# Performance work log

Measured on AMD Instinct MI355X. Metric: run time of the kernel, lower is better.

## Reference

```python
import jax, jax.numpy as jnp
import numpy as np

IN_F, OUT_F, NB = 4096, 4096, 8
BS = IN_F // NB  # 512


def setup_inputs() -> dict:
    key = jax.random.key(0)
    k1, k2, k3, k4 = jax.random.split(key, 4)
    weight = jax.random.normal(k1, (OUT_F, IN_F), dtype=jnp.float32) * 0.02
    bias = jax.random.normal(k2, (OUT_F,), dtype=jnp.float32) * 0.02
    x = jax.random.normal(k3, (4, 2048, IN_F), dtype=jnp.float32)
    R_blocks = jax.random.normal(k4, (NB, BS, BS), dtype=jnp.float32) * 0.1
    return {"weight": weight, "bias": bias, "x": x, "R_blocks": R_blocks, "layer_idx": 0}


def cayley_transform(A):
    # A: [nb, bs, bs]; Q = (I - A_skew) @ inv(I + A_skew + 1e-6 I)
    bs = A.shape[-1]
    I = jnp.eye(bs, dtype=A.dtype)
    A_skew = 0.5 * (A - jnp.swapaxes(A, -2, -1))
    return jnp.matmul(I - A_skew, jnp.linalg.inv(I + A_skew + 1e-6 * I))


def reference(weight, bias, x, R_blocks, layer_idx):
    R_ortho = cayley_transform(R_blocks)  # [nb, bs, bs]
    # weight @ block_diag(R) == per-block contraction on the in_features axis
    w = weight.reshape(OUT_F, NB, BS)
    tw = jnp.einsum('onb,nbc->onc', w, R_ortho).reshape(OUT_F, IN_F)
    # F.linear: x @ tw.T + bias
    out = jnp.einsum('bsi,oi->bso', x, tw) + bias
    return out
```

## Files before the change

kernel.cpp:

```cpp
#include <hip/hip_runtime.h>
#include <hip/hip_bf16.h>


typedef unsigned short u16;
typedef __attribute__((ext_vector_type(8))) __bf16 bf16x8;
typedef __attribute__((ext_vector_type(4))) float f32x4;
typedef __attribute__((ext_vector_type(8))) unsigned short u16x8;
typedef __attribute__((ext_vector_type(4))) unsigned short u16x4;

#define C0   1.000001f
#define C1Q  2.000001f
#define AS1 __attribute__((address_space(1)))
#define AS3 __attribute__((address_space(3)))

__device__ __forceinline__ u16 f2bf(float x) {
  union { float f; unsigned u; } v; v.f = x;
  return (u16)((v.u + 0x7fffu + ((v.u >> 16) & 1u)) >> 16);
}
__device__ __forceinline__ float bf2f(u16 h) {
  union { float f; unsigned u; } v; v.u = ((unsigned)h) << 16; return v.f;
}

__device__ __forceinline__ void get_coefs(float t, float* C) {
  float lam = powf(t, 0.25f);
  float a = 2.0f / (C0 * C0 + lam);
  float e = (lam - C0 * C0) / (lam + C0 * C0);
  float sq = e * e, c1 = 2.0f / (2.0f - sq);
  C[0] = a; C[1] = 2.0f * c1; C[2] = -c1 * a;
  C[3] = 2.0f * c1 * a; C[4] = -c1 * a * a;
  e = sq / (2.0f - sq); sq = e * e;
  float c2 = 2.0f / (2.0f - sq);
  C[5] = 2.0f * c2; C[6] = -c2;
  e = sq / (2.0f - sq); sq = e * e;
  float c3 = 2.0f / (2.0f - sq);
  C[7] = 2.0f * c3; C[8] = -c3;
}

__global__ __launch_bounds__(256) void k_build_M(const float* __restrict__ R,
                                                 u16* __restrict__ Mh,
                                                 u16* __restrict__ Ml) {
  __shared__ float t1[32][33];
  const int n = blockIdx.z;
  const int tr = blockIdx.y * 32, tc = blockIdx.x * 32;
  const int ly = threadIdx.x >> 5, lx = threadIdx.x & 31;
  const float* Rb = R + (size_t)n * 262144;
  float a[4];
#pragma unroll
  for (int i = 0; i < 4; ++i) {
    a[i] = Rb[(size_t)(tr + ly + i * 8) * 512 + tc + lx];
    t1[ly + i * 8][lx] = Rb[(size_t)(tc + ly + i * 8) * 512 + tr + lx];
  }
  __syncthreads();
#pragma unroll
  for (int i = 0; i < 4; ++i) {
    const int r = tr + ly + i * 8, c = tc + lx;
    float m = 0.5f * (a[i] - t1[lx][ly + i * 8]) + (r == c ? C0 : 0.0f);
    u16 h = f2bf(m);
    const size_t idx = (size_t)n * 262144 + (size_t)r * 512 + c;
    Mh[idx] = h;
    Ml[idx] = f2bf(m - bf2f(h));
  }
}

__global__ __launch_bounds__(256) void k_init(const u16* __restrict__ Mh,
                                              const u16* __restrict__ Ml,
                                              const u16* __restrict__ G,
                                              const u16* __restrict__ G2,
                                              const u16* __restrict__ H,
                                              const float* __restrict__ part,
                                              float* __restrict__ coef,
                                              u16* __restrict__ X1,
                                              u16* __restrict__ T2) {
  __shared__ float sp[64];
  __shared__ float sc[13];
  const int n = blockIdx.x >> 7;
  if (threadIdx.x < 64) sp[threadIdx.x] = part[n * 64 + threadIdx.x];
  __syncthreads();
  if (threadIdx.x == 0) {
    float s = 0.f;
    for (int i = 0; i < 64; ++i) s += sp[i];
    float C[9];
    get_coefs(s, C);
#pragma unroll
    for (int k = 0; k < 9; ++k) sc[k] = C[k];
    sc[9]  = 2.0f * C0 * C[3];
    sc[10] = -C[3];
    sc[11] = 2.0f * C0 * C[4];
    sc[12] = -C[4];
    coef[n] = C[0];
    coef[8 + n]  = C[1]; coef[16 + n] = C[2];
    coef[24 + n] = C[3]; coef[32 + n] = C[4];
    coef[40 + n] = C[5]; coef[48 + n] = C[6];
    coef[56 + n] = C[7]; coef[64 + n] = C[8];
  }
  __syncthreads();
  const size_t base = ((size_t)blockIdx.x * 256 + threadIdx.x) * 8;
  const int r  = (int)((base >> 9) & 511);
  const int c0 = (int)(base & 511);
  u16x8 mh = *reinterpret_cast<const u16x8*>(Mh + base);
  u16x8 ml = *reinterpret_cast<const u16x8*>(Ml + base);
  u16x8 g  = *reinterpret_cast<const u16x8*>(G  + base);
  u16x8 g2 = *reinterpret_cast<const u16x8*>(G2 + base);
  u16x8 hh = *reinterpret_cast<const u16x8*>(H  + base);
  u16x8 x1, t2;
#pragma unroll
  for (int e = 0; e < 8; ++e) {
    float m = bf2f(mh[e]) + bf2f(ml[e]);
    float gv = bf2f(g[e]);
    x1[e] = f2bf((r == c0 + e ? sc[9] : 0.0f) + sc[10] * m + sc[11] * gv +
                 sc[12] * bf2f(hh[e]));
    t2[e] = f2bf(sc[3] * gv + sc[4] * bf2f(g2[e]));
  }
  *reinterpret_cast<u16x8*>(X1 + base) = x1;
  *reinterpret_cast<u16x8*>(T2 + base) = t2;
}

#define BMM_FRAGS(rs)                                                          \
  bf16x8 a[2], b[2], al2[2], bl2[2];                                           \
  _Pragma("unroll")                                                            \
  for (int i = 0; i < 2; ++i) {                                                \
    const int fr = wr * 32 + i * 16 + c15;                                     \
    const int ia = (rs) * 2048 + fr * 32 + ((lk ^ (fr & 3)) * 8);              \
    a[i] = *reinterpret_cast<const bf16x8*>(&sA[ia]);                          \
    if constexpr (PROD3) al2[i] = *reinterpret_cast<const bf16x8*>(&sAl[ia]);  \
  }                                                                            \
  _Pragma("unroll")                                                            \
  for (int j = 0; j < 2; ++j) {                                                \
    const int fc = wc * 32 + j * 16 + c15;                                     \
    const int ib = (rs) * 2048 + fc * 32 + ((lk ^ (fc & 3)) * 8);              \
    b[j] = *reinterpret_cast<const bf16x8*>(&sB[ib]);                          \
    if constexpr (PROD3) bl2[j] = *reinterpret_cast<const bf16x8*>(&sBl[ib]);  \
  }                                                                            \
  _Pragma("unroll")                                                            \
  for (int i = 0; i < 2; ++i)                                                  \
    _Pragma("unroll")                                                          \
    for (int j = 0; j < 2; ++j) {                                              \
      acc[i][j] = __builtin_amdgcn_mfma_f32_16x16x32_bf16(a[i], b[j], acc[i][j], 0, 0, 0); \
      if constexpr (PROD3) {                                                   \
        acc[i][j] = __builtin_amdgcn_mfma_f32_16x16x32_bf16(a[i],   bl2[j], acc[i][j], 0, 0, 0); \
        acc[i][j] = __builtin_amdgcn_mfma_f32_16x16x32_bf16(al2[i], b[j],   acc[i][j], 0, 0, 0); \
      }                                                                        \
    }

#define BMM_WAIT(SEL)                                                          \
  if ((SEL) == 0) {                                                            \
    if constexpr (PROD3) asm volatile("s_waitcnt vmcnt(12)" ::: "memory");     \
    else                 asm volatile("s_waitcnt vmcnt(6)" ::: "memory");      \
  } else if ((SEL) == 1) {                                                     \
    if constexpr (PROD3) asm volatile("s_waitcnt vmcnt(8)" ::: "memory");      \
    else                 asm volatile("s_waitcnt vmcnt(4)" ::: "memory");      \
  } else if ((SEL) == 2) {                                                     \
    if constexpr (PROD3) asm volatile("s_waitcnt vmcnt(4)" ::: "memory");      \
    else                 asm volatile("s_waitcnt vmcnt(2)" ::: "memory");      \
  } else {                                                                     \
    asm volatile("s_waitcnt vmcnt(0)" ::: "memory");                           \
  }

template <int PROD3, int DMODE, int OMODE, int DUAL, int FROB, int VOUT = 0>
__global__ __launch_bounds__(256)
void k_bmm(const u16* __restrict__ Ah, const u16* __restrict__ Al,
           const u16* __restrict__ Bh, const u16* __restrict__ Bl,
           const u16* __restrict__ Dh, const u16* __restrict__ Dl,
           u16* __restrict__ Cnh, u16* __restrict__ Cnl,
           u16* __restrict__ Cth, u16* __restrict__ Ctl,
           float cd, float cs,
           const float* __restrict__ cdp, const float* __restrict__ csp,
           const float* __restrict__ cvsrc, u16* __restrict__ cvdst, int zmm,
           const u16* __restrict__ A2, const u16* __restrict__ B2,
           const u16* __restrict__ D2, u16* __restrict__ C2,
           float* __restrict__ part) {
  __shared__ __align__(16) u16 sA[5 * 2048], sB[5 * 2048];
  __shared__ __align__(16) u16 sAl[PROD3 ? 5 * 2048 : 8];
  __shared__ __align__(16) u16 sBl[PROD3 ? 5 * 2048 : 8];
  __shared__ float fred[FROB ? 4 : 1];

  if ((int)blockIdx.z >= zmm) {
    const int zi = ((int)blockIdx.z - zmm) * 64 + blockIdx.y * 8 + blockIdx.x;
    const int chunk = zi >> 7;
    const int base = (zi & 127) * 256 + (int)threadIdx.x;
    const float* src = cvsrc + (size_t)chunk * 4194304;
    u16* dst = cvdst + (size_t)chunk * 4194304;
#pragma unroll
    for (int e = 0; e < 16; ++e) {
      const size_t g = (size_t)(base + e * 32768) * 8;
      float4 f0 = *reinterpret_cast<const float4*>(src + g);
      float4 f1 = *reinterpret_cast<const float4*>(src + g + 4);
      u16x8 w;
      w[0] = f2bf(f0.x); w[1] = f2bf(f0.y); w[2] = f2bf(f0.z); w[3] = f2bf(f0.w);
      w[4] = f2bf(f1.x); w[5] = f2bf(f1.y); w[6] = f2bf(f1.z); w[7] = f2bf(f1.w);
      *reinterpret_cast<u16x8*>(dst + g) = w;
    }
    return;
  }

  const int zq = DUAL ? ((blockIdx.z >> 3) & 1) : 0;
  const u16* Ah_ = (DUAL && zq) ? A2 : Ah;
  const u16* Bh_ = (DUAL && zq) ? B2 : Bh;
  const u16* Dh_ = (DUAL && zq) ? D2 : Dh;
  u16* Cnh_ = (DUAL && zq) ? C2 : Cnh;
  const size_t zb = (size_t)(blockIdx.z & 7) * 262144;
  const int tid = threadIdx.x, lane = tid & 63, wave = tid >> 6;
  const int m0 = blockIdx.y * 64, n0 = blockIdx.x * 64;
  const int wr = wave >> 1, wc = wave & 1;
  const int c15 = lane & 15, lk = lane >> 4;
  const int srow = tid >> 2;
  const int sg = (tid & 3) ^ (srow & 3);
  f32x4 acc[2][2] = {};
  const u16* pa = Ah_ + zb + (size_t)(m0 + srow) * 512 + sg * 8;
  const u16* pb = Bh_ + zb + (size_t)(n0 + srow) * 512 + sg * 8;
  const u16* pal = PROD3 ? Al + zb + (size_t)(m0 + srow) * 512 + sg * 8 : pa;
  const u16* pbl = PROD3 ? Bl + zb + (size_t)(n0 + srow) * 512 + sg * 8 : pb;

  int jn = 0, js = 0;
  auto STG = [&]() {
    if (jn < 16) {
      const int off = jn << 5;
      __builtin_amdgcn_global_load_lds((const AS1 void*)(pa + off),
                                       (AS3 void*)(sA + js * 2048 + tid * 8), 16, 0, 0);
      __builtin_amdgcn_global_load_lds((const AS1 void*)(pb + off),
                                       (AS3 void*)(sB + js * 2048 + tid * 8), 16, 0, 0);
      if constexpr (PROD3) {
        __builtin_amdgcn_global_load_lds((const AS1 void*)(pal + off),
                                         (AS3 void*)(sAl + js * 2048 + tid * 8), 16, 0, 0);
        __builtin_amdgcn_global_load_lds((const AS1 void*)(pbl + off),
                                         (AS3 void*)(sBl + js * 2048 + tid * 8), 16, 0, 0);
      }
    }
    ++jn; js = (js == 4) ? 0 : js + 1;
  };

  STG(); STG(); STG();
  int rs = 0;
  for (int t = 0; t < 13; ++t) {
    STG();
    BMM_WAIT(0)
    __builtin_amdgcn_s_barrier();
    BMM_FRAGS(rs)
    rs = (rs == 4) ? 0 : rs + 1;
  }
  STG();
  BMM_WAIT(1)
  __builtin_amdgcn_s_barrier();
  { BMM_FRAGS(rs) }
  rs = (rs == 4) ? 0 : rs + 1;
  STG();
  BMM_WAIT(2)
  __builtin_amdgcn_s_barrier();
  { BMM_FRAGS(rs) }
  rs = (rs == 4) ? 0 : rs + 1;
  STG();
  BMM_WAIT(3)
  __builtin_amdgcn_s_barrier();
  { BMM_FRAGS(rs) }

  const float cdL = cdp ? cdp[blockIdx.z & 7] : cd;
  const float csL = csp ? csp[blockIdx.z & 7] : cs;
  float fs = 0.f;
#pragma unroll
  for (int i = 0; i < 2; ++i)
#pragma unroll
    for (int j = 0; j < 2; ++j) {
      const int rowb = m0 + wr * 32 + i * 16 + lk * 4;
      const int col  = n0 + wc * 32 + j * 16 + c15;
      u16 hv[4], lv[4];
#pragma unroll
      for (int r = 0; r < 4; ++r) {
        float val = csL * acc[i][j][r];
        float dv = 0.f;
        if constexpr (DMODE >= 1) {
          dv = bf2f(Dh_[zb + (size_t)(rowb + r) * 512 + col]);
          if constexpr (DMODE == 2) dv += bf2f(Dl[zb + (size_t)(rowb + r) * 512 + col]);
        }
        float nval, tval;
        if constexpr (VOUT) { tval = val; nval = cdL * dv - val; }
        else { nval = tval = val + cdL * dv; }
        u16 nh = f2bf(nval);
        if constexpr (OMODE & 1) Cnh_[zb + (size_t)(rowb + r) * 512 + col] = nh;
        if constexpr (FROB) { float v = bf2f(nh); fs += v * v; }
        if constexpr (OMODE & 2)
          Cnl[zb + (size_t)(rowb + r) * 512 + col] = f2bf(nval - bf2f(nh));
        if constexpr (OMODE & 12) {
          u16 th = f2bf(tval);
          hv[r] = th;
          if constexpr (OMODE & 8) lv[r] = f2bf(tval - bf2f(th));
        }
      }
      if constexpr (OMODE & 4) {
        u16x4 v; v[0] = hv[0]; v[1] = hv[1]; v[2] = hv[2]; v[3] = hv[3];
        *reinterpret_cast<u16x4*>(&Cth[zb + (size_t)col * 512 + rowb]) = v;
      }
      if constexpr (OMODE & 8) {
        u16x4 v; v[0] = lv[0]; v[1] = lv[1]; v[2] = lv[2]; v[3] = lv[3];
        *reinterpret_cast<u16x4*>(&Ctl[zb + (size_t)col * 512 + rowb]) = v;
      }
    }
  if constexpr (FROB) {
    for (int off = 32; off; off >>= 1) fs += __shfl_down(fs, off, 64);
    if ((tid & 63) == 0) fred[tid >> 6] = fs;
    __syncthreads();
    if (tid == 0 && (int)blockIdx.z < 8)
      part[(blockIdx.z & 7) * 64 + blockIdx.y * 8 + blockIdx.x] =
          fred[0] + fred[1] + fred[2] + fred[3];
  }
}

__global__ __launch_bounds__(256)
void k_twmm(const u16* __restrict__ W, const u16* __restrict__ Qt,
            u16* __restrict__ tw) {
  __shared__ __align__(16) u16 sA[5 * 2048], sB[5 * 2048];
  const int z = blockIdx.z;
  const size_t zb = (size_t)z * 262144;
  const int tid = threadIdx.x, lane = tid & 63, wave = tid >> 6;
  const int m0 = blockIdx.y * 64, n0 = blockIdx.x * 64;
  const int wr = wave >> 1, wc = wave & 1;
  const int c15 = lane & 15, lk = lane >> 4;
  const int srow = tid >> 2;
  const int sg = (tid & 3) ^ (srow & 3);
  f32x4 acc[2][2] = {};
  const u16* pa = W + (size_t)(m0 + srow) * 4096 + z * 512 + sg * 8;
  const u16* pb = Qt + zb + (size_t)(n0 + srow) * 512 + sg * 8;

  int jn = 0, js = 0;
  auto STG = [&]() {
    if (jn < 16) {
      const int off = jn << 5;
      __builtin_amdgcn_global_load_lds((const AS1 void*)(pa + off),
                                       (AS3 void*)(sA + js * 2048 + tid * 8), 16, 0, 0);
      __builtin_amdgcn_global_load_lds((const AS1 void*)(pb + off),
                                       (AS3 void*)(sB + js * 2048 + tid * 8), 16, 0, 0);
    }
    ++jn; js = (js == 4) ? 0 : js + 1;
  };

#define TW_FRAGS(rs)                                                           \
  {                                                                            \
    bf16x8 a[2], b[2];                                                         \
    _Pragma("unroll")                                                          \
    for (int i = 0; i < 2; ++i) {                                              \
      const int fr = wr * 32 + i * 16 + c15;                                   \
      a[i] = *reinterpret_cast<const bf16x8*>(                                 \
          &sA[(rs) * 2048 + fr * 32 + ((lk ^ (fr & 3)) * 8)]);                 \
    }                                                                          \
    _Pragma("unroll")                                                          \
    for (int j = 0; j < 2; ++j) {                                              \
      const int fc = wc * 32 + j * 16 + c15;                                   \
      b[j] = *reinterpret_cast<const bf16x8*>(                                 \
          &sB[(rs) * 2048 + fc * 32 + ((lk ^ (fc & 3)) * 8)]);                 \
    }                                                                          \
    _Pragma("unroll")                                                          \
    for (int i = 0; i < 2; ++i)                                                \
      _Pragma("unroll")                                                        \
      for (int j = 0; j < 2; ++j)                                              \
        acc[i][j] = __builtin_amdgcn_mfma_f32_16x16x32_bf16(a[i], b[j], acc[i][j], 0, 0, 0); \
  }

  STG(); STG(); STG();
  int rs = 0;
  for (int t = 0; t < 13; ++t) {
    STG();
    asm volatile("s_waitcnt vmcnt(6)" ::: "memory");
    __builtin_amdgcn_s_barrier();
    TW_FRAGS(rs)
    rs = (rs == 4) ? 0 : rs + 1;
  }
  STG();
  asm volatile("s_waitcnt vmcnt(4)" ::: "memory");
  __builtin_amdgcn_s_barrier();
  TW_FRAGS(rs)
  rs = (rs == 4) ? 0 : rs + 1;
  STG();
  asm volatile("s_waitcnt vmcnt(2)" ::: "memory");
  __builtin_amdgcn_s_barrier();
  TW_FRAGS(rs)
  rs = (rs == 4) ? 0 : rs + 1;
  STG();
  asm volatile("s_waitcnt vmcnt(0)" ::: "memory");
  __builtin_amdgcn_s_barrier();
  TW_FRAGS(rs)

#pragma unroll
  for (int i = 0; i < 2; ++i)
#pragma unroll
    for (int j = 0; j < 2; ++j) {
      const int rowb = m0 + wr * 32 + i * 16 + lk * 4;
      const int col  = z * 512 + n0 + wc * 32 + j * 16 + c15;
#pragma unroll
      for (int r = 0; r < 4; ++r)
        tw[(size_t)(rowb + r) * 4096 + col] = f2bf(acc[i][j][r]);
    }
}

#define NSL 18

#define RD_A3(dst, MH)                                                         \
  _Pragma("unroll")                                                            \
  for (int m = 0; m < 4; ++m)                                                  \
    dst[m] = *reinterpret_cast<const bf16x8*>(                                 \
        &lds[aslot * 4096 + ((MH) * 64 + m * 16 + c15) * 32 + gsw * 8]);

#define RD_B3(dst)                                                             \
  _Pragma("unroll")                                                            \
  for (int n = 0; n < 4; ++n)                                                  \
    dst[n] = *reinterpret_cast<const bf16x8*>(                                 \
        &lds[bslot * 4096 + (bq64 + n * 16 + c15) * 32 + gsw * 8]);

#define MFMA16(afX, bfX, MH)                                                   \
  __builtin_amdgcn_s_setprio(1);                                               \
  _Pragma("unroll")                                                            \
  for (int m = 0; m < 4; ++m)                                                  \
    _Pragma("unroll")                                                          \
    for (int n = 0; n < 4; ++n)                                                \
      acc[(MH) * 4 + m][n] = __builtin_amdgcn_mfma_f32_16x16x32_bf16(          \
          afX[m], bfX[n], acc[(MH) * 4 + m][n], 0, 0, 0);                      \
  __builtin_amdgcn_s_setprio(0);

#define TILE32(WM)                                                             \
  {                                                                            \
    int aslot = s0 + wr;            if (aslot >= NSL) aslot -= NSL;            \
    int bslot = s0 + 2 + (wc >> 1); if (bslot >= NSL) bslot -= NSL;            \
    STAGE(); STAGE();                                                          \
    RD_B3(bfr)                                                                 \
    RD_A3(afA, 0)                                                              \
    MFMA16(afA, bfr, 0)                                                        \
    STAGE(); STAGE();                                                          \
    RD_A3(afB, 1)                                                              \
    MFMA16(afB, bfr, 1)                                                        \
    if ((WM) == 1) asm volatile("s_waitcnt vmcnt(8)" ::: "memory");            \
    if ((WM) == 2) asm volatile("s_waitcnt vmcnt(4)" ::: "memory");            \
    if ((WM) == 3) asm volatile("s_waitcnt vmcnt(0)" ::: "memory");            \
    if ((WM) != 0) {                                                           \
      __builtin_amdgcn_s_barrier();                                            \
      __builtin_amdgcn_sched_barrier(0);                                       \
    }                                                                          \
    s0 += 4; if (s0 >= NSL) s0 -= NSL;                                         \
  }

__global__ __launch_bounds__(512, 2)
void k_gemm256(const u16* __restrict__ A, const u16* __restrict__ B,
               const float* __restrict__ bias,
               float* __restrict__ C, int N, int K) {
  __shared__ __align__(16) u16 lds[NSL * 4096];
  const int tid = threadIdx.x, lane = tid & 63, wave = tid >> 6;
  int bid = blockIdx.y * gridDim.x + blockIdx.x;
  const int cpx = (gridDim.x * gridDim.y) >> 3;
  bid = (bid & 7) * cpx + (bid >> 3);
  const int nbx = N >> 8;
  const int bx = bid % nbx, by = bid / nbx;
  const int m0 = by << 8, n0 = bx << 8;
  const int wr = wave >> 2, wc = wave & 3;
  const int srow = tid >> 2;
  const int sgc  = (tid & 3) ^ ((srow >> 1) & 3);
  const int c15 = lane & 15, lq = lane >> 4;
  const int gsw = lq ^ ((c15 >> 1) & 3);
  const int bq64 = (wc & 1) * 64;
  const int NT = K >> 5;

  f32x4 acc[8][4] = {};
  bf16x8 afA[4], afB[4], bfr[4];

  int jn = 0, js = 0;
  auto STAGE = [&]() {
    if (jn < 4 * NT) {
      const int t = jn >> 2, q = jn & 3;
      const u16* srcb = (q < 2)
          ? A + (size_t)(m0 + q * 128 + srow) * (size_t)K
          : B + (size_t)(n0 + (q - 2) * 128 + srow) * (size_t)K;
      const u16* src = srcb + (t << 5) + sgc * 8;
      u16* dst = (u16*)lds + js * 4096 + tid * 8;
      __builtin_amdgcn_global_load_lds(
          (const AS1 void*)src, (AS3 void*)dst, 16, 0, 0);
    }
    ++jn; js = (js == NSL - 1) ? 0 : js + 1;
  };

#pragma unroll
  for (int i = 0; i < 12; ++i) STAGE();
  asm volatile("s_waitcnt vmcnt(8)" ::: "memory");
  __builtin_amdgcn_s_barrier();
  __builtin_amdgcn_sched_barrier(0);

  int s0 = 0;
  for (int tau = 0; tau < NT - 3; ++tau) {
    TILE32(1)
  }
  TILE32(2)
  TILE32(3)
  TILE32(0)

#pragma unroll
  for (int n = 0; n < 4; ++n) {
    const int col = n0 + wc * 64 + n * 16 + c15;
    const float bv = bias[col];
#pragma unroll
    for (int mi = 0; mi < 8; ++mi) {
      const int rowb = m0 + wr * 128 + mi * 16 + (lq << 2);
#pragma unroll
      for (int r = 0; r < 4; ++r)
        C[(size_t)(rowb + r) * N + col] = acc[mi][n][r] + bv;
    }
  }
}

extern "C" void kernel_launch(void* const* d_in, const int* in_sizes, int n_in,
                              void* d_out, int out_size, void* d_ws, size_t ws_size,
                              hipStream_t stream) {
  const float* W    = (const float*)d_in[0];
  const float* bias = (const float*)d_in[1];
  const float* x    = (const float*)d_in[2];
  const float* R    = (const float*)d_in[3];
  float* out = (float*)d_out;

  char* ws = (char*)d_ws;
  u16* x_bf = (u16*)(ws);
  u16* tw   = (u16*)(ws + 67108864);
  u16* W_bf = (u16*)(ws + 100663296);

  char* arena = (char*)d_out;
  auto slot = [&](int i) -> u16* { return (u16*)(arena + (size_t)i * 4194304); };
  u16 *Mh = slot(0), *Ml = slot(1);
  u16 *G = slot(2), *G2 = slot(3), *H = slot(4);
  u16 *T2 = slot(6), *X1 = slot(7), *X2 = slot(8), *T3 = slot(9);
  u16 *X3h = slot(10), *X3l = slot(11), *X3th = slot(12), *X3tl = slot(13);
  u16 *Tpth = slot(14), *Tptl = slot(15);
  u16 *Vh = slot(16), *Vl = slot(17);
  u16 *Qt = slot(20);
  float* coef = (float*)(arena + (size_t)21 * 4194304);
  float* part = coef + 1024;

  const u16* NUL = nullptr;
  const float* NULF = nullptr;
  u16* NULW = nullptr;
  float* NULP = nullptr;
  const dim3 gC2(8, 8, 12);
  const dim3 gD2(8, 8, 20);

  k_build_M<<<dim3(16, 16, 8), 256, 0, stream>>>(R, Mh, Ml);
  k_bmm<0, 0, 1, 0, 0><<<gC2, 256, 0, stream>>>(Mh, NUL, Mh, NUL, NUL, NUL,
      G, NULW, NULW, NULW, 0.f, 1.f, NULF, NULF, W, W_bf, 8,
      NUL, NUL, NUL, NULW, NULP);
  k_bmm<0, 0, 1, 1, 1><<<gD2, 256, 0, stream>>>(G, NUL, G, NUL, NUL, NUL,
      G2, NULW, NULW, NULW, 0.f, 1.f, NULF, NULF,
      W + (size_t)2 * 4194304, W_bf + (size_t)2 * 4194304, 16,
      Mh, G, NUL, H, part);
  k_init<<<1024, 256, 0, stream>>>(Mh, Ml, G, G2, H, part, coef, X1, T2);
  k_bmm<0, 1, 1, 1, 0><<<gD2, 256, 0, stream>>>(X1, NUL, T2, NUL, X1, NUL,
      X2, NULW, NULW, NULW, 0.f, 0.f, coef + 40, coef + 48,
      x, x_bf, 16, T2, T2, T2, T3, NULP);
  k_bmm<0, 1, 15, 0, 0><<<gC2, 256, 0, stream>>>(X2, NUL, T3, NUL, X2, NUL,
      X3h, X3l, X3th, X3tl, 0.f, 0.f, coef + 56, coef + 64,
      x + (size_t)2 * 4194304, x_bf + (size_t)2 * 4194304, 8,
      NUL, NUL, NUL, NULW, NULP);
  k_bmm<1, 2, 15, 0, 0, 1><<<gC2, 256, 0, stream>>>(Mh, Ml, X3th, X3tl,
      X3h, X3l, Vh, Vl, Tpth, Tptl, C1Q, 1.f, NULF, NULF,
      x + (size_t)4 * 4194304, x_bf + (size_t)4 * 4194304, 8,
      NUL, NUL, NUL, NULW, NULP);
  k_bmm<1, 2, 4, 0, 0><<<gC2, 256, 0, stream>>>(Vh, Vl, Tpth, Tptl, Vh, Vl,
      NULW, NULW, Qt, NULW, 2.f, -1.f, NULF, NULF,
      x + (size_t)6 * 4194304, x_bf + (size_t)6 * 4194304, 8,
      NUL, NUL, NUL, NULW, NULP);
  k_twmm<<<dim3(8, 64, 8), 256, 0, stream>>>(W_bf, Qt, tw);
  k_gemm256<<<dim3(16, 32), 512, 0, stream>>>(x_bf, tw, bias, out, 4096, 4096);
}
```

Measured before the change: 467.8 us.

## Fuse build_M and first Gram-chain matmuls into one persistent kernel with grid barriers

Replaces the M-building kernel and two batched matmul launches with a single 512-block persistent kernel. It builds M, computes G=M·M, G2=G·G and H=M·G, and converts W to bf16, using software grid barriers built on atomics between phases. The goal is to remove launch gaps and tail effects between these small dependent stages. The risk is that the grid barrier requires all 512 blocks to be co-resident (launch bounds allow 2 per CU), and the new 64x64 tile matmul may be less efficient than the old k_bmm.

```diff
diff --git a/kernel.cpp b/kernel.cpp
--- a/kernel.cpp
+++ b/kernel.cpp
@@ -12,6 +12,7 @@
 #define C1Q  2.000001f
 #define AS1 __attribute__((address_space(1)))
 #define AS3 __attribute__((address_space(3)))
+#define NBLK 512
 
 __device__ __forceinline__ u16 f2bf(float x) {
   union { float f; unsigned u; } v; v.f = x;
@@ -19,6 +20,28 @@
 }
 __device__ __forceinline__ float bf2f(u16 h) {
   union { float f; unsigned u; } v; v.u = ((unsigned)h) << 16; return v.f;
+}
+
+__device__ __forceinline__ void grid_sync(unsigned* bar) {
+  __syncthreads();
+  if (threadIdx.x == 0) {
+    __threadfence();
+    unsigned g = __hip_atomic_load(bar + 1, __ATOMIC_RELAXED,
+                                   __HIP_MEMORY_SCOPE_AGENT);
+    unsigned a = __hip_atomic_fetch_add(bar, 1u, __ATOMIC_ACQ_REL,
+                                        __HIP_MEMORY_SCOPE_AGENT);
+    if (a == NBLK - 1u) {
+      __hip_atomic_store(bar, 0u, __ATOMIC_RELAXED, __HIP_MEMORY_SCOPE_AGENT);
+      __hip_atomic_store(bar + 1, g + 1u, __ATOMIC_RELEASE,
+                         __HIP_MEMORY_SCOPE_AGENT);
+    } else {
+      while (__hip_atomic_load(bar + 1, __ATOMIC_ACQUIRE,
+                               __HIP_MEMORY_SCOPE_AGENT) == g)
+        __builtin_amdgcn_s_sleep(1);
+    }
+    __threadfence();
+  }
+  __syncthreads();
 }
 
 __device__ __forceinline__ void get_coefs(float t, float* C) {
@@ -36,30 +59,143 @@
   C[7] = 2.0f * c3; C[8] = -c3;
 }
 
-__global__ __launch_bounds__(256) void k_build_M(const float* __restrict__ R,
-                                                 u16* __restrict__ Mh,
-                                                 u16* __restrict__ Ml) {
+__device__ void mm64(int tile, const u16* __restrict__ Ah,
+                     const u16* __restrict__ Bh, u16* __restrict__ Cnh,
+                     int frob, u16* sA, u16* sB, float* fred,
+                     float* __restrict__ part) {
+  const int tid = threadIdx.x;
+  const int z = tile >> 6, tl = tile & 63;
+  const size_t zb = (size_t)z * 262144;
+  const int m0 = (tl >> 3) * 64, n0 = (tl & 7) * 64;
+  const int lane = tid & 63, wave = tid >> 6;
+  const int wr = wave >> 1, wc = wave & 1;
+  const int c15 = lane & 15, lk = lane >> 4;
+  const int srow = tid >> 2, sg = (tid & 3) ^ (srow & 3);
+  f32x4 acc[2][2] = {};
+  const u16* pa = Ah + zb + (size_t)(m0 + srow) * 512 + sg * 8;
+  const u16* pb = Bh + zb + (size_t)(n0 + srow) * 512 + sg * 8;
+
+  int jn = 0, js = 0;
+  auto STG = [&]() {
+    if (jn < 16) {
+      const int off = jn << 5;
+      __builtin_amdgcn_global_load_lds((const AS1 void*)(pa + off),
+                                       (AS3 void*)(sA + js * 2048 + tid * 8), 16, 0, 0);
+      __builtin_amdgcn_global_load_lds((const AS1 void*)(pb + off),
+                                       (AS3 void*)(sB + js * 2048 + tid * 8), 16, 0, 0);
+    }
+    ++jn; js = (js == 4) ? 0 : js + 1;
+  };
+
+  STG(); STG(); STG();
+  int rs = 0;
+  for (int t = 0; t < 16; ++t) {
+    STG();
+    if (t < 13)      asm volatile("s_waitcnt vmcnt(6)" ::: "memory");
+    else if (t == 13) asm volatile("s_waitcnt vmcnt(4)" ::: "memory");
+    else if (t == 14) asm volatile("s_waitcnt vmcnt(2)" ::: "memory");
+    else              asm volatile("s_waitcnt vmcnt(0)" ::: "memory");
+    __builtin_amdgcn_s_barrier();
+    bf16x8 a2[2], b2[2];
+#pragma unroll
+    for (int i = 0; i < 2; ++i) {
+      const int fr = wr * 32 + i * 16 + c15;
+      a2[i] = *reinterpret_cast<const bf16x8*>(
+          &sA[rs * 2048 + fr * 32 + ((lk ^ (fr & 3)) * 8)]);
+    }
+#pragma unroll
+    for (int j = 0; j < 2; ++j) {
+      const int fc = wc * 32 + j * 16 + c15;
+      b2[j] = *reinterpret_cast<const bf16x8*>(
+          &sB[rs * 2048 + fc * 32 + ((lk ^ (fc & 3)) * 8)]);
+    }
+#pragma unroll
+    for (int i = 0; i < 2; ++i)
+#pragma unroll
+      for (int j = 0; j < 2; ++j)
+        acc[i][j] = __builtin_amdgcn_mfma_f32_16x16x32_bf16(a2[i], b2[j], acc[i][j], 0, 0, 0);
+    rs = (rs == 4) ? 0 : rs + 1;
+  }
+  float fs = 0.f;
+#pragma unroll
+  for (int i = 0; i < 2; ++i)
+#pragma unroll
+    for (int j = 0; j < 2; ++j) {
+      const int rowb = m0 + wr * 32 + i * 16 + lk * 4;
+      const int col  = n0 + wc * 32 + j * 16 + c15;
+#pragma unroll
+      for (int r = 0; r < 4; ++r) {
+        u16 h = f2bf(acc[i][j][r]);
+        Cnh[zb + (size_t)(rowb + r) * 512 + col] = h;
+        if (frob) { float v = bf2f(h); fs += v * v; }
+      }
+    }
+  if (frob) {
+    for (int off = 32; off; off >>= 1) fs += __shfl_down(fs, off, 64);
+    if ((tid & 63) == 0) fred[tid >> 6] = fs;
+    __syncthreads();
+    if (tid == 0) part[tile] = fred[0] + fred[1] + fred[2] + fred[3];
+    __syncthreads();
+  }
+}
+
+__device__ __forceinline__ void conv16k(const float* __restrict__ src,
+                                        u16* __restrict__ dst) {
+  const size_t base = (size_t)blockIdx.x * 16384;
+#pragma unroll
+  for (int g = 0; g < 8; ++g) {
+    const size_t off = base + g * 2048 + (size_t)threadIdx.x * 8;
+    float4 f0 = *reinterpret_cast<const float4*>(src + off);
+    float4 f1 = *reinterpret_cast<const float4*>(src + off + 4);
+    u16x8 w;
+    w[0] = f2bf(f0.x); w[1] = f2bf(f0.y); w[2] = f2bf(f0.z); w[3] = f2bf(f0.w);
+    w[4] = f2bf(f1.x); w[5] = f2bf(f1.y); w[6] = f2bf(f1.z); w[7] = f2bf(f1.w);
+    *reinterpret_cast<u16x8*>(dst + off) = w;
+  }
+}
+
+__global__ __launch_bounds__(256, 2)
+void k_chain1(const float* __restrict__ R, const float* __restrict__ W,
+              u16* Mh, u16* Ml, u16* G, u16* G2, u16* H,
+              u16* W_bf, float* part, unsigned* bar) {
+  __shared__ __align__(16) u16 sA[5 * 2048], sB[5 * 2048];
   __shared__ float t1[32][33];
-  const int n = blockIdx.z;
-  const int tr = blockIdx.y * 32, tc = blockIdx.x * 32;
-  const int ly = threadIdx.x >> 5, lx = threadIdx.x & 31;
-  const float* Rb = R + (size_t)n * 262144;
-  float a[4];
-#pragma unroll
-  for (int i = 0; i < 4; ++i) {
-    a[i] = Rb[(size_t)(tr + ly + i * 8) * 512 + tc + lx];
-    t1[ly + i * 8][lx] = Rb[(size_t)(tc + ly + i * 8) * 512 + tr + lx];
-  }
+  __shared__ float fred[4];
+  const int bid = blockIdx.x, tid = threadIdx.x;
+
+  {
+    const int ly = tid >> 5, lx = tid & 31;
+    for (int i4 = 0; i4 < 4; ++i4) {
+      const int t = bid * 4 + i4;
+      const int n = t >> 8, rem = t & 255;
+      const int tr = (rem >> 4) * 32, tc = (rem & 15) * 32;
+      const float* Rb = R + (size_t)n * 262144;
+      float a[4];
+#pragma unroll
+      for (int i = 0; i < 4; ++i) {
+        a[i] = Rb[(size_t)(tr + ly + i * 8) * 512 + tc + lx];
+        t1[ly + i * 8][lx] = Rb[(size_t)(tc + ly + i * 8) * 512 + tr + lx];
+      }
+      __syncthreads();
+#pragma unroll
+      for (int i = 0; i < 4; ++i) {
+        const int r = tr + ly + i * 8, c = tc + lx;
+        float m = 0.5f * (a[i] - t1[lx][ly + i * 8]) + (r == c ? C0 : 0.0f);
+        u16 h = f2bf(m);
+        const size_t idx = (size_t)n * 262144 + (size_t)r * 512 + c;
+        Mh[idx] = h; Ml[idx] = f2bf(m - bf2f(h));
+      }
+      __syncthreads();
+    }
+  }
+  grid_sync(bar);
+  mm64(bid, Mh, Mh, G, 0, sA, sB, fred, part);
+  conv16k(W, W_bf);
+  grid_sync(bar);
+  mm64(bid, G, G, G2, 1, sA, sB, fred, part);
   __syncthreads();
-#pragma unroll
-  for (int i = 0; i < 4; ++i) {
-    const int r = tr + ly + i * 8, c = tc + lx;
-    float m = 0.5f * (a[i] - t1[lx][ly + i * 8]) + (r == c ? C0 : 0.0f);
-    u16 h = f2bf(m);
-    const size_t idx = (size_t)n * 262144 + (size_t)r * 512 + c;
-    Mh[idx] = h;
-    Ml[idx] = f2bf(m - bf2f(h));
-  }
+  mm64(bid, Mh, G, H, 0, sA, sB, fred, part);
+  conv16k(W + 8388608, W_bf + 8388608);
 }
 
 __global__ __launch_bounds__(256) void k_init(const u16* __restrict__ Mh,
@@ -526,6 +662,7 @@
   u16 *Qt = slot(20);
   float* coef = (float*)(arena + (size_t)21 * 4194304);
   float* part = coef + 1024;
+  unsigned* bar = (unsigned*)(arena + (size_t)22 * 4194304);
 
   const u16* NUL = nullptr;
   const float* NULF = nullptr;
@@ -534,14 +671,9 @@
   const dim3 gC2(8, 8, 12);
   const dim3 gD2(8, 8, 20);
 
-  k_build_M<<<dim3(16, 16, 8), 256, 0, stream>>>(R, Mh, Ml);
-  k_bmm<0, 0, 1, 0, 0><<<gC2, 256, 0, stream>>>(Mh, NUL, Mh, NUL, NUL, NUL,
-      G, NULW, NULW, NULW, 0.f, 1.f, NULF, NULF, W, W_bf, 8,
-      NUL, NUL, NUL, NULW, NULP);
-  k_bmm<0, 0, 1, 1, 1><<<gD2, 256, 0, stream>>>(G, NUL, G, NUL, NUL, NUL,
-      G2, NULW, NULW, NULW, 0.f, 1.f, NULF, NULF,
-      W + (size_t)2 * 4194304, W_bf + (size_t)2 * 4194304, 16,
-      Mh, G, NUL, H, part);
+  hipMemsetAsync(bar, 0, 64, stream);
+  k_chain1<<<dim3(NBLK), 256, 0, stream>>>(R, W, Mh, Ml, G, G2, H,
+                                           W_bf, part, bar);
   k_init<<<1024, 256, 0, stream>>>(Mh, Ml, G, G2, H, part, coef, X1, T2);
   k_bmm<0, 1, 1, 1, 0><<<gD2, 256, 0, stream>>>(X1, NUL, T2, NUL, X1, NUL,
       X2, NULW, NULW, NULW, 0.f, 0.f, coef + 40, coef + 48,
```

After: 668.6 us. 1.43x slower.
